# Optimization experiments

Hardware: AMD Instinct MI355X
Metric: run time of the kernel (lower is better)

The kernel has to match this reference:

```python
import math
import jax, jax.numpy as jnp
import numpy as np

B, N = 1, 512
C_S, C_Z, H, C, P_Q, P_V = 384, 128, 12, 16, 4, 8
CAT = C_Z * H + C * H + 3 * H * P_V + 1  # 2017


def _apply(t_r, t_t, x):
    # t_r: (b,n,3,3), t_t: (b,n,3), x: (b,3,h,p,n) -> global frame coords
    xg = jnp.einsum('bnij,bjhpn->bihpn', t_r, x)
    return xg + jnp.swapaxes(t_t, 1, 2)[:, :, None, None, :]


def setup_inputs() -> dict:
    key = jax.random.key(0)
    ks = jax.random.split(key, 14)
    f = lambda k, shp: jax.random.normal(k, shp, dtype=jnp.float32)
    return {
        's': f(ks[0], (B, C_S, N)),
        'z': f(ks[1], (B, C_Z, N, N)),
        't_r': f(ks[2], (B, N, 3, 3)),
        't_t': f(ks[3], (B, N, 3)),
        'Wq': f(ks[4], (C * H, C_S)) * 0.02,
        'Wk': f(ks[5], (C * H, C_S)) * 0.02,
        'Wv': f(ks[6], (C * H, C_S)) * 0.02,
        'Wqp': f(ks[7], (3 * H * P_Q, C_S)) * 0.02,
        'Wkp': f(ks[8], (3 * H * P_Q, C_S)) * 0.02,
        'Wvp': f(ks[9], (3 * H * P_V, C_S)) * 0.02,
        'Wb': f(ks[10], (H, C_Z)) * 0.02,
        'gamma': f(ks[11], (H, 1, 1)) * 0.5,
        'Ws': f(ks[12], (C_S, CAT)) * 0.02,
        'bs': jnp.zeros((C_S,), dtype=jnp.float32),
    }


def reference(s, z, t_r, t_t, Wq, Wk, Wv, Wqp, Wkp, Wvp, Wb, gamma, Ws, bs):
    b, _, n = s.shape
    w_c = math.sqrt(2.0 / (9.0 * P_Q))
    w_l = math.sqrt(1.0 / 3.0)

    proj = lambda W: jnp.einsum('oc,bcn->bon', W, s)
    # torch rearrange 'b (c h) i -> b c h i' == reshape(b, c, h, n)
    q = proj(Wq).reshape(b, C, H, n)
    k = proj(Wk).reshape(b, C, H, n)
    v = proj(Wv).reshape(b, C, H, n)
    qp = proj(Wqp).reshape(b, 3, H, P_Q, n)
    kp = proj(Wkp).reshape(b, 3, H, P_Q, n)
    vp = proj(Wvp).reshape(b, 3, H, P_V, n)

    qg = _apply(t_r, t_t, qp)  # (b,3,h,p,n)
    kg = _apply(t_r, t_t, kp)
    diff = qg[..., :, None] - kg[..., None, :]          # (b,3,h,p,n,n)
    dist2 = jnp.sum(diff * diff, axis=(1, 3))           # sum coords + points -> (b,h,n,n)
    tmp = jax.nn.softplus(gamma)[None] * (w_c / 2.0) * dist2

    b_bias = jnp.einsum('hc,bcij->bhij', Wb, z)
    qk = jnp.einsum('bchi,bchj->bhij', q, k) / math.sqrt(C)
    a = jax.nn.softmax(w_l * (qk + b_bias - tmp), axis=-1)  # (b,h,n,n)

    o1 = jnp.einsum('bhij,bcij->bchi', a, z).reshape(b, C_Z * H, n)
    o2 = jnp.einsum('bhij,bchj->bchi', a, v).reshape(b, C * H, n)

    vg = _apply(t_r, t_t, vp)                           # (b,3,h,pv,n)
    o3g = jnp.einsum('bhij,bchpj->bchpi', a, vg)        # (b,3,h,pv,n)
    t_r_inv = jnp.swapaxes(t_r, -1, -2)
    t_t_inv = jnp.einsum('bnij,bnj->bni', -t_r_inv, t_t)
    o3 = _apply(t_r_inv, t_t_inv, o3g).reshape(b, 3 * H * P_V, n)
    o3_norm = jnp.linalg.norm(o3, axis=1, keepdims=True)  # (b,1,n)

    cat = jnp.concatenate([o1, o2, o3, o3_norm], axis=1)  # (b, CAT, n)
    return jnp.einsum('oc,bcn->bon', Ws, cat) + bs[None, :, None]
```

## Files before the change

### kernel.cpp

```cpp
#include <hip/hip_runtime.h>
#include <math.h>

#define N 512
#define H 12
#define CC 16
#define CZ 128
#define CS 384
#define PQ 4
#define PV 8
#define CATR 2017

__global__ __launch_bounds__(256) void k_proj(
    const float* __restrict__ s,
    const float* __restrict__ Wq, const float* __restrict__ Wk, const float* __restrict__ Wv,
    const float* __restrict__ Wqp, const float* __restrict__ Wkp, const float* __restrict__ Wvp,
    float* __restrict__ proj)
{
    __shared__ float Wt[16][33];
    __shared__ float St[32][128];
    int t = threadIdx.x;
    int o0 = blockIdx.x * 16;
    int n0 = blockIdx.y * 128;
    const float* Wsrc; int orow;
    if (o0 < 192)      { Wsrc = Wq;  orow = o0; }
    else if (o0 < 384) { Wsrc = Wk;  orow = o0-192; }
    else if (o0 < 576) { Wsrc = Wv;  orow = o0-384; }
    else if (o0 < 720) { Wsrc = Wqp; orow = o0-576; }
    else if (o0 < 864) { Wsrc = Wkp; orow = o0-720; }
    else               { Wsrc = Wvp; orow = o0-864; }

    int og = t >> 6, nl = t & 63;
    float acc[4][2] = {};
    for (int c0 = 0; c0 < CS; c0 += 32) {
        __syncthreads();
        for (int k = 0; k < 2; k++) {
            int idx = t + k*256;
            int oo = idx >> 5, ccol = idx & 31;
            Wt[oo][ccol] = Wsrc[(orow+oo)*CS + c0 + ccol];
        }
        for (int k = 0; k < 4; k++) {
            int idx = t + k*256;
            int ccr = idx >> 5, nn4 = idx & 31;
            float4 v = *(const float4*)&s[(c0+ccr)*N + n0 + nn4*4];
            *(float4*)&St[ccr][nn4*4] = v;
        }
        __syncthreads();
        for (int kk = 0; kk < 32; kk++) {
            float sv0 = St[kk][nl], sv1 = St[kk][nl+64];
            #pragma unroll
            for (int r = 0; r < 4; r++) {
                float w = Wt[og*4+r][kk];
                acc[r][0] += w * sv0;
                acc[r][1] += w * sv1;
            }
        }
    }
    for (int r = 0; r < 4; r++) {
        int o = o0 + og*4 + r;
        proj[o*N + n0 + nl]      = acc[r][0];
        proj[o*N + n0 + 64 + nl] = acc[r][1];
    }
}

__global__ void k_frames(const float* __restrict__ proj,
                         const float* __restrict__ t_r, const float* __restrict__ t_t,
                         float* __restrict__ qg, float* __restrict__ kg, float* __restrict__ vg)
{
    int gid = blockIdx.x * blockDim.x + threadIdx.x;
    int n = gid & (N-1);
    int hp = gid >> 9;
    if (hp >= 192) return;
    const float* src; float* dst; int rowb, stride;
    if (hp < 48)      { src = proj + 576*N; dst = qg; rowb = hp;    stride = 48; }
    else if (hp < 96) { src = proj + 720*N; dst = kg; rowb = hp-48; stride = 48; }
    else              { src = proj + 864*N; dst = vg; rowb = hp-96; stride = 96; }
    float x0 = src[(rowb + 0*stride)*N + n];
    float x1 = src[(rowb + 1*stride)*N + n];
    float x2 = src[(rowb + 2*stride)*N + n];
    #pragma unroll
    for (int d = 0; d < 3; d++) {
        float r0 = t_r[(n*3+d)*3+0], r1 = t_r[(n*3+d)*3+1], r2 = t_r[(n*3+d)*3+2];
        dst[(rowb + d*stride)*N + n] = r0*x0 + r1*x1 + r2*x2 + t_t[n*3+d];
    }
}

__global__ void k_sq(const float* __restrict__ qg, const float* __restrict__ kg,
                     float* __restrict__ sq_q, float* __restrict__ sq_k)
{
    int gid = blockIdx.x * blockDim.x + threadIdx.x;
    int n = gid & (N-1);
    int sel = gid >> 9;
    int h = sel % H;
    const float* g = (sel < H) ? qg : kg;
    float* outp = (sel < H) ? sq_q : sq_k;
    float acc = 0.f;
    #pragma unroll
    for (int d = 0; d < 3; d++)
        #pragma unroll
        for (int p = 0; p < PQ; p++) {
            float v = g[(size_t)((d*H + h)*PQ + p)*N + n];
            acc += v*v;
        }
    outp[h*N + n] = acc;
}

__global__ __launch_bounds__(256) void k_logits(
    const float* __restrict__ z, const float* __restrict__ proj,
    const float* __restrict__ qg, const float* __restrict__ kg,
    const float* __restrict__ sq_q, const float* __restrict__ sq_k,
    const float* __restrict__ Wb, const float* __restrict__ gamma,
    float* __restrict__ a)
{
    __shared__ float red[12*2*256];
    int i = blockIdx.x;
    int jc = blockIdx.y;
    int t = threadIdx.x;
    int jl = t & 63;
    int cgu = __builtin_amdgcn_readfirstlane(t >> 6);
    int j = jc*256 + jl*4;
    const size_t NN = (size_t)N*N;
    const float w_l  = 0.57735026918962584f;
    const float w_c2 = 0.11785113019775793f;

    float ch[12];
    #pragma unroll
    for (int h = 0; h < 12; h++) {
        float g = gamma[h];
        float sp = (g > 20.f) ? g : log1pf(expf(g));
        ch[h] = sp * w_c2;
    }

    float acc[12][4] = {};

    {
        const float* zp = z + (size_t)(cgu*32)*NN + (size_t)i*N + j;
        for (int cc = 0; cc < 32; cc += 8) {
            float4 zb[8];
            #pragma unroll
            for (int u = 0; u < 8; u++)
                zb[u] = *(const float4*)(zp + (size_t)(cc+u)*NN);
            #pragma unroll
            for (int u = 0; u < 8; u++) {
                int c = cgu*32 + cc + u;
                #pragma unroll
                for (int h = 0; h < 12; h++) {
                    float w = Wb[h*CZ + c];
                    acc[h][0] += w*zb[u].x; acc[h][1] += w*zb[u].y;
                    acc[h][2] += w*zb[u].z; acc[h][3] += w*zb[u].w;
                }
            }
        }
    }
    {
        const float* q  = proj;
        const float* kk = proj + 192*N;
        #pragma unroll
        for (int cc = 0; cc < 4; cc++) {
            int c = cgu*4 + cc;
            #pragma unroll
            for (int h = 0; h < 12; h++) {
                int r = c*12 + h;
                float qv = 0.25f * q[(size_t)r*N + i];
                float4 k4 = *(const float4*)&kk[(size_t)r*N + j];
                acc[h][0] += qv*k4.x; acc[h][1] += qv*k4.y;
                acc[h][2] += qv*k4.z; acc[h][3] += qv*k4.w;
            }
        }
    }
    {
        #pragma unroll
        for (int dd = 0; dd < 3; dd++) {
            int dp = cgu*3 + dd; int d = dp >> 2, p = dp & 3;
            #pragma unroll
            for (int h = 0; h < 12; h++) {
                int r = (d*12 + h)*4 + p;
                float qv = 2.f * ch[h] * qg[(size_t)r*N + i];
                float4 k4 = *(const float4*)&kg[(size_t)r*N + j];
                acc[h][0] += qv*k4.x; acc[h][1] += qv*k4.y;
                acc[h][2] += qv*k4.z; acc[h][3] += qv*k4.w;
            }
        }
    }

    if (cgu >= 2) {
        #pragma unroll
        for (int h = 0; h < 12; h++) {
            float4 v; v.x=acc[h][0]; v.y=acc[h][1]; v.z=acc[h][2]; v.w=acc[h][3];
            *(float4*)&red[(h*2 + (cgu-2))*256 + jl*4] = v;
        }
    }
    __syncthreads();
    if (cgu < 2) {
        #pragma unroll
        for (int h = 0; h < 12; h++) {
            float4 o = *(const float4*)&red[(h*2 + cgu)*256 + jl*4];
            acc[h][0] += o.x; acc[h][1] += o.y; acc[h][2] += o.z; acc[h][3] += o.w;
        }
        if (cgu == 1) {
            #pragma unroll
            for (int h = 0; h < 12; h++) {
                float4 v; v.x=acc[h][0]; v.y=acc[h][1]; v.z=acc[h][2]; v.w=acc[h][3];
                *(float4*)&red[(h*2 + 1)*256 + jl*4] = v;
            }
        }
    }
    __syncthreads();
    if (cgu == 0) {
        #pragma unroll
        for (int h = 0; h < 12; h++) {
            float4 o = *(const float4*)&red[(h*2 + 1)*256 + jl*4];
            float s0 = sq_q[h*N + i];
            float4 sk = *(const float4*)&sq_k[h*N + j];
            float4 r;
            r.x = w_l*(acc[h][0] + o.x - ch[h]*(s0 + sk.x));
            r.y = w_l*(acc[h][1] + o.y - ch[h]*(s0 + sk.y));
            r.z = w_l*(acc[h][2] + o.z - ch[h]*(s0 + sk.z));
            r.w = w_l*(acc[h][3] + o.w - ch[h]*(s0 + sk.w));
            *(float4*)&a[((size_t)h*N + i)*N + j] = r;
        }
    }
}

__global__ __launch_bounds__(256) void k_softmax(float* __restrict__ a)
{
    int r = blockIdx.x*4 + (threadIdx.x >> 6);
    int l = threadIdx.x & 63;
    float* row = a + (size_t)r*N + l*8;
    float4 v0 = *(const float4*)row;
    float4 v1 = *(const float4*)(row + 4);
    float m = fmaxf(fmaxf(fmaxf(v0.x,v0.y),fmaxf(v0.z,v0.w)),
                    fmaxf(fmaxf(v1.x,v1.y),fmaxf(v1.z,v1.w)));
    for (int s = 32; s > 0; s >>= 1) m = fmaxf(m, __shfl_xor(m, s));
    v0.x = __expf(v0.x-m); v0.y = __expf(v0.y-m);
    v0.z = __expf(v0.z-m); v0.w = __expf(v0.w-m);
    v1.x = __expf(v1.x-m); v1.y = __expf(v1.y-m);
    v1.z = __expf(v1.z-m); v1.w = __expf(v1.w-m);
    float sm = v0.x+v0.y+v0.z+v0.w+v1.x+v1.y+v1.z+v1.w;
    for (int s = 32; s > 0; s >>= 1) sm += __shfl_xor(sm, s);
    float inv = 1.f/sm;
    v0.x*=inv; v0.y*=inv; v0.z*=inv; v0.w*=inv;
    v1.x*=inv; v1.y*=inv; v1.z*=inv; v1.w*=inv;
    *(float4*)row = v0;
    *(float4*)(row+4) = v1;
}

__global__ __launch_bounds__(256) void k_o1(
    const float* __restrict__ z, const float* __restrict__ a, float* __restrict__ cat)
{
    __shared__ float als[12*516];
    __shared__ float zls[64*68];
    int i = blockIdx.x;
    int c0 = blockIdx.y * 64;
    int t = threadIdx.x;
    int cg = t & 31, hg = (t>>5)&1, jq = t>>6;

    #pragma unroll
    for (int k = 0; k < 6; k++) {
        int idx = t + k*256;
        int h = idx >> 7, j4 = idx & 127;
        *(float4*)&als[h*516 + j4*4] = *(const float4*)&a[((size_t)h*N + i)*N + j4*4];
    }
    float acc[2][6] = {};
    for (int jc = 0; jc < 8; jc++) {
        __syncthreads();
        #pragma unroll
        for (int k = 0; k < 4; k++) {
            int idx = t + k*256;
            int c = idx >> 4, j4 = idx & 15;
            *(float4*)&zls[c*68 + j4*4] =
                *(const float4*)&z[((size_t)(c0+c)*N + i)*N + jc*64 + j4*4];
        }
        __syncthreads();
        #pragma unroll
        for (int s = 0; s < 4; s++) {
            int jo = jq*16 + s*4;
            float4 z0 = *(const float4*)&zls[cg*68 + jo];
            float4 z1 = *(const float4*)&zls[(cg+32)*68 + jo];
            #pragma unroll
            for (int hh = 0; hh < 6; hh++) {
                float4 a4 = *(const float4*)&als[(hg*6+hh)*516 + jc*64 + jo];
                acc[0][hh] += z0.x*a4.x + z0.y*a4.y + z0.z*a4.z + z0.w*a4.w;
                acc[1][hh] += z1.x*a4.x + z1.y*a4.y + z1.z*a4.z + z1.w*a4.w;
            }
        }
    }
    __syncthreads();
    if (jq >= 2) {
        float* rb = &zls[((jq-2)*128 + (t & 127))*13];
        #pragma unroll
        for (int r = 0; r < 2; r++)
            #pragma unroll
            for (int hh = 0; hh < 6; hh++) rb[r*6+hh] = acc[r][hh];
    }
    __syncthreads();
    if (jq < 2) {
        const float* rb = &zls[(jq*128 + (t & 127))*13];
        #pragma unroll
        for (int r = 0; r < 2; r++)
            #pragma unroll
            for (int hh = 0; hh < 6; hh++) acc[r][hh] += rb[r*6+hh];
        if (jq == 1) {
            float* rb2 = &als[(t & 63)*13];
            #pragma unroll
            for (int r = 0; r < 2; r++)
                #pragma unroll
                for (int hh = 0; hh < 6; hh++) rb2[r*6+hh] = acc[r][hh];
        }
    }
    __syncthreads();
    if (jq == 0) {
        const float* rb2 = &als[t*13];
        #pragma unroll
        for (int r = 0; r < 2; r++)
            #pragma unroll
            for (int hh = 0; hh < 6; hh++) {
                float v = acc[r][hh] + rb2[r*6+hh];
                int c = c0 + cg + 32*r;
                int h = hg*6 + hh;
                cat[(size_t)(c*H + h)*N + i] = v;
            }
    }
}

__global__ __launch_bounds__(256) void k_o2o3g(
    const float* __restrict__ a, const float* __restrict__ proj, const float* __restrict__ vg,
    float* __restrict__ cat, float* __restrict__ o3g)
{
    __shared__ float ats[8*132];
    __shared__ float vts[40*132];
    int h = blockIdx.x, i0 = blockIdx.y*8;
    int t = threadIdx.x;
    int il = t & 7, rg = (t>>3)&7, jq = t>>6;
    const float* v = proj + 384*N;
    float acc[5] = {};
    for (int jc = 0; jc < 4; jc++) {
        __syncthreads();
        {
            int ii = t >> 5, j4 = t & 31;
            *(float4*)&ats[ii*132 + j4*4] =
                *(const float4*)&a[((size_t)h*N + i0+ii)*N + jc*128 + j4*4];
        }
        #pragma unroll
        for (int k = 0; k < 5; k++) {
            int idx = t + k*256;
            int r = idx >> 5, j4 = idx & 31;
            const float* src = (r < 16) ? (v + (size_t)(r*H + h)*N)
                : (vg + (size_t)(((r-16)>>3)*96 + h*PV + ((r-16)&7))*N);
            *(float4*)&vts[r*132 + j4*4] = *(const float4*)&src[jc*128 + j4*4];
        }
        __syncthreads();
        #pragma unroll
        for (int s = 0; s < 8; s++) {
            int jo = jq*32 + s*4;
            float4 a4 = *(const float4*)&ats[il*132 + jo];
            #pragma unroll
            for (int r = 0; r < 5; r++) {
                float4 v4 = *(const float4*)&vts[(rg*5+r)*132 + jo];
                acc[r] += v4.x*a4.x + v4.y*a4.y + v4.z*a4.z + v4.w*a4.w;
            }
        }
    }
    __syncthreads();
    if (jq >= 2) {
        float* rb = &ats[((jq-2)*64 + (t & 63))*5];
        #pragma unroll
        for (int r = 0; r < 5; r++) rb[r] = acc[r];
    }
    __syncthreads();
    if (jq < 2) {
        const float* rb = &ats[(jq*64 + (t & 63))*5];
        #pragma unroll
        for (int r = 0; r < 5; r++) acc[r] += rb[r];
        if (jq == 1) {
            float* rb2 = &ats[640 + (t & 63)*5];
            #pragma unroll
            for (int r = 0; r < 5; r++) rb2[r] = acc[r];
        }
    }
    __syncthreads();
    if (jq == 0) {
        const float* rb2 = &ats[640 + t*5];
        #pragma unroll
        for (int r = 0; r < 5; r++) {
            float val = acc[r] + rb2[r];
            int row = rg*5 + r;
            if (row < 16) cat[(size_t)(1536 + row*H + h)*N + i0 + il] = val;
            else { int rr = row - 16;
                   o3g[(size_t)((rr>>3)*96 + h*PV + (rr&7))*N + i0 + il] = val; }
        }
    }
}

__global__ void k_o3(const float* __restrict__ o3g,
                     const float* __restrict__ t_r, const float* __restrict__ t_t,
                     float* __restrict__ cat)
{
    int gid = blockIdx.x*blockDim.x + threadIdx.x;
    int i = gid & (N-1), hp = gid >> 9;
    if (hp >= 96) return;
    float x0 = o3g[(size_t)(0*96 + hp)*N + i] - t_t[i*3+0];
    float x1 = o3g[(size_t)(1*96 + hp)*N + i] - t_t[i*3+1];
    float x2 = o3g[(size_t)(2*96 + hp)*N + i] - t_t[i*3+2];
    #pragma unroll
    for (int d = 0; d < 3; d++) {
        float o = t_r[(i*3+0)*3+d]*x0 + t_r[(i*3+1)*3+d]*x1 + t_r[(i*3+2)*3+d]*x2;
        cat[(size_t)(1728 + d*96 + hp)*N + i] = o;
    }
}

__global__ void k_norm(float* __restrict__ cat)
{
    int i = blockIdx.x*blockDim.x + threadIdx.x;
    if (i >= N) return;
    float acc = 0.f;
    for (int r = 0; r < 288; r++) {
        float v = cat[(size_t)(1728+r)*N + i];
        acc += v*v;
    }
    cat[(size_t)2016*N + i] = sqrtf(acc);
}

__global__ __launch_bounds__(256) void k_final(
    const float* __restrict__ Ws, const float* __restrict__ bs,
    const float* __restrict__ cat, float* __restrict__ out)
{
    __shared__ float Wt[16*33];
    __shared__ float Ct[32*66];
    int o0 = blockIdx.x*16, n0 = blockIdx.y*64;
    int ks = blockIdx.z;
    int kbeg = ks*505, kend = min(CATR, kbeg+505);
    int t = threadIdx.x;
    int og = t >> 6, nl = t & 63;
    float acc[4] = {};
    for (int c0 = kbeg; c0 < kend; c0 += 32) {
        __syncthreads();
        for (int k = 0; k < 2; k++) {
            int idx = t + k*256;
            int oo = idx >> 5, ccol = idx & 31;
            int c = c0 + ccol;
            Wt[oo*33 + ccol] = (c < kend) ? Ws[(size_t)(o0+oo)*CATR + c] : 0.f;
        }
        for (int k = 0; k < 4; k++) {
            int idx = t + k*256;
            int ccr = idx >> 5, j2 = idx & 31;
            int c = c0 + ccr;
            float2 vv; vv.x = 0.f; vv.y = 0.f;
            if (c < kend) vv = *(const float2*)&cat[(size_t)c*N + n0 + j2*2];
            *(float2*)&Ct[ccr*66 + j2*2] = vv;
        }
        __syncthreads();
        int klim = min(32, kend - c0);
        for (int kk = 0; kk < klim; kk++) {
            float cv = Ct[kk*66 + nl];
            #pragma unroll
            for (int r = 0; r < 4; r++)
                acc[r] += Wt[(og*4+r)*33 + kk] * cv;
        }
    }
    #pragma unroll
    for (int r = 0; r < 4; r++) {
        int o = o0 + og*4 + r;
        float val = acc[r];
        if (ks == 0) val += bs[o];
        atomicAdd(&out[(size_t)o*N + n0 + nl], val);
    }
}

extern "C" void kernel_launch(void* const* d_in, const int* in_sizes, int n_in,
                              void* d_out, int out_size, void* d_ws, size_t ws_size,
                              hipStream_t stream)
{
    const float* s     = (const float*)d_in[0];
    const float* z     = (const float*)d_in[1];
    const float* t_r   = (const float*)d_in[2];
    const float* t_t   = (const float*)d_in[3];
    const float* Wq    = (const float*)d_in[4];
    const float* Wk    = (const float*)d_in[5];
    const float* Wv    = (const float*)d_in[6];
    const float* Wqp   = (const float*)d_in[7];
    const float* Wkp   = (const float*)d_in[8];
    const float* Wvp   = (const float*)d_in[9];
    const float* Wb    = (const float*)d_in[10];
    const float* gamma = (const float*)d_in[11];
    const float* Ws    = (const float*)d_in[12];
    const float* bs    = (const float*)d_in[13];
    float* out = (float*)d_out;

    float* ws   = (float*)d_ws;
    float* proj = ws;
    float* qg   = proj + 1152*N;
    float* kg   = qg   + 144*N;
    float* vg   = kg   + 144*N;
    float* sq_q = vg   + 288*N;
    float* sq_k = sq_q + H*N;
    float* o3g  = sq_k + H*N;
    float* a    = o3g  + 288*N;
    float* cat  = a    + (size_t)H*N*N;

    k_proj   <<<dim3(72,4),   256, 0, stream>>>(s, Wq, Wk, Wv, Wqp, Wkp, Wvp, proj);
    k_frames <<<384,          256, 0, stream>>>(proj, t_r, t_t, qg, kg, vg);
    k_sq     <<<48,           256, 0, stream>>>(qg, kg, sq_q, sq_k);
    k_logits <<<dim3(512,2),  256, 0, stream>>>(z, proj, qg, kg, sq_q, sq_k, Wb, gamma, a);
    k_softmax<<<1536,         256, 0, stream>>>(a);
    k_o1     <<<dim3(512,2),  256, 0, stream>>>(z, a, cat);
    k_o2o3g  <<<dim3(12,64),  256, 0, stream>>>(a, proj, vg, cat, o3g);
    k_o3     <<<192,          256, 0, stream>>>(o3g, t_r, t_t, cat);
    k_norm   <<<2,            256, 0, stream>>>(cat);
    hipMemsetAsync(out, 0, (size_t)CS*N*sizeof(float), stream);
    k_final  <<<dim3(24,8,4), 256, 0, stream>>>(Ws, bs, cat, out);
}
```

Baseline: 418.2 us.

## Fuse logits, softmax and z-weighted output into one per-row kernel

```diff
diff --git a/kernel.cpp b/kernel.cpp
--- a/kernel.cpp
+++ b/kernel.cpp
@@ -104,20 +104,19 @@
     outp[h*N + n] = acc;
 }
 
-__global__ __launch_bounds__(256) void k_logits(
+__global__ __launch_bounds__(256) void k_attn_o1(
     const float* __restrict__ z, const float* __restrict__ proj,
     const float* __restrict__ qg, const float* __restrict__ kg,
     const float* __restrict__ sq_q, const float* __restrict__ sq_k,
     const float* __restrict__ Wb, const float* __restrict__ gamma,
-    float* __restrict__ a)
-{
-    __shared__ float red[12*2*256];
+    float* __restrict__ a, float* __restrict__ cat)
+{
+    __shared__ float als[12*516];
+    __shared__ float zls[128*68];
     int i = blockIdx.x;
-    int jc = blockIdx.y;
     int t = threadIdx.x;
     int jl = t & 63;
     int cgu = __builtin_amdgcn_readfirstlane(t >> 6);
-    int j = jc*256 + jl*4;
     const size_t NN = (size_t)N*N;
     const float w_l  = 0.57735026918962584f;
     const float w_c2 = 0.11785113019775793f;
@@ -130,192 +129,189 @@
         ch[h] = sp * w_c2;
     }
 
-    float acc[12][4] = {};
-
-    {
-        const float* zp = z + (size_t)(cgu*32)*NN + (size_t)i*N + j;
-        for (int cc = 0; cc < 32; cc += 8) {
-            float4 zb[8];
-            #pragma unroll
-            for (int u = 0; u < 8; u++)
-                zb[u] = *(const float4*)(zp + (size_t)(cc+u)*NN);
-            #pragma unroll
-            for (int u = 0; u < 8; u++) {
-                int c = cgu*32 + cc + u;
+    for (int jc = 0; jc < 2; jc++) {
+        int j = jc*256 + jl*4;
+        float acc[12][4] = {};
+
+        {
+            const float* zp = z + (size_t)(cgu*32)*NN + (size_t)i*N + j;
+            for (int cc = 0; cc < 32; cc += 8) {
+                float4 zb[8];
+                #pragma unroll
+                for (int u = 0; u < 8; u++)
+                    zb[u] = *(const float4*)(zp + (size_t)(cc+u)*NN);
+                #pragma unroll
+                for (int u = 0; u < 8; u++) {
+                    int c = cgu*32 + cc + u;
+                    #pragma unroll
+                    for (int h = 0; h < 12; h++) {
+                        float w = Wb[h*CZ + c];
+                        acc[h][0] += w*zb[u].x; acc[h][1] += w*zb[u].y;
+                        acc[h][2] += w*zb[u].z; acc[h][3] += w*zb[u].w;
+                    }
+                }
+            }
+        }
+        {
+            const float* q  = proj;
+            const float* kk = proj + 192*N;
+            #pragma unroll
+            for (int cc = 0; cc < 4; cc++) {
+                int c = cgu*4 + cc;
                 #pragma unroll
                 for (int h = 0; h < 12; h++) {
-                    float w = Wb[h*CZ + c];
-                    acc[h][0] += w*zb[u].x; acc[h][1] += w*zb[u].y;
-                    acc[h][2] += w*zb[u].z; acc[h][3] += w*zb[u].w;
+                    int r = c*12 + h;
+                    float qv = 0.25f * q[(size_t)r*N + i];
+                    float4 k4 = *(const float4*)&kk[(size_t)r*N + j];
+                    acc[h][0] += qv*k4.x; acc[h][1] += qv*k4.y;
+                    acc[h][2] += qv*k4.z; acc[h][3] += qv*k4.w;
                 }
             }
         }
-    }
-    {
-        const float* q  = proj;
-        const float* kk = proj + 192*N;
-        #pragma unroll
-        for (int cc = 0; cc < 4; cc++) {
-            int c = cgu*4 + cc;
-            #pragma unroll
-            for (int h = 0; h < 12; h++) {
-                int r = c*12 + h;
-                float qv = 0.25f * q[(size_t)r*N + i];
-                float4 k4 = *(const float4*)&kk[(size_t)r*N + j];
-                acc[h][0] += qv*k4.x; acc[h][1] += qv*k4.y;
-                acc[h][2] += qv*k4.z; acc[h][3] += qv*k4.w;
-            }
-        }
-    }
-    {
-        #pragma unroll
-        for (int dd = 0; dd < 3; dd++) {
-            int dp = cgu*3 + dd; int d = dp >> 2, p = dp & 3;
-            #pragma unroll
-            for (int h = 0; h < 12; h++) {
-                int r = (d*12 + h)*4 + p;
-                float qv = 2.f * ch[h] * qg[(size_t)r*N + i];
-                float4 k4 = *(const float4*)&kg[(size_t)r*N + j];
-                acc[h][0] += qv*k4.x; acc[h][1] += qv*k4.y;
-                acc[h][2] += qv*k4.z; acc[h][3] += qv*k4.w;
-            }
-        }
-    }
-
-    if (cgu >= 2) {
-        #pragma unroll
-        for (int h = 0; h < 12; h++) {
-            float4 v; v.x=acc[h][0]; v.y=acc[h][1]; v.z=acc[h][2]; v.w=acc[h][3];
-            *(float4*)&red[(h*2 + (cgu-2))*256 + jl*4] = v;
-        }
-    }
-    __syncthreads();
-    if (cgu < 2) {
-        #pragma unroll
-        for (int h = 0; h < 12; h++) {
-            float4 o = *(const float4*)&red[(h*2 + cgu)*256 + jl*4];
-            acc[h][0] += o.x; acc[h][1] += o.y; acc[h][2] += o.z; acc[h][3] += o.w;
-        }
-        if (cgu == 1) {
+        {
+            #pragma unroll
+            for (int dd = 0; dd < 3; dd++) {
+                int dp = cgu*3 + dd; int d = dp >> 2, p = dp & 3;
+                #pragma unroll
+                for (int h = 0; h < 12; h++) {
+                    int r = (d*12 + h)*4 + p;
+                    float qv = 2.f * ch[h] * qg[(size_t)r*N + i];
+                    float4 k4 = *(const float4*)&kg[(size_t)r*N + j];
+                    acc[h][0] += qv*k4.x; acc[h][1] += qv*k4.y;
+                    acc[h][2] += qv*k4.z; acc[h][3] += qv*k4.w;
+                }
+            }
+        }
+
+        __syncthreads();
+        float* red = zls;
+        if (cgu >= 2) {
             #pragma unroll
             for (int h = 0; h < 12; h++) {
                 float4 v; v.x=acc[h][0]; v.y=acc[h][1]; v.z=acc[h][2]; v.w=acc[h][3];
-                *(float4*)&red[(h*2 + 1)*256 + jl*4] = v;
-            }
-        }
-    }
-    __syncthreads();
-    if (cgu == 0) {
-        #pragma unroll
-        for (int h = 0; h < 12; h++) {
-            float4 o = *(const float4*)&red[(h*2 + 1)*256 + jl*4];
-            float s0 = sq_q[h*N + i];
-            float4 sk = *(const float4*)&sq_k[h*N + j];
-            float4 r;
-            r.x = w_l*(acc[h][0] + o.x - ch[h]*(s0 + sk.x));
-            r.y = w_l*(acc[h][1] + o.y - ch[h]*(s0 + sk.y));
-            r.z = w_l*(acc[h][2] + o.z - ch[h]*(s0 + sk.z));
-            r.w = w_l*(acc[h][3] + o.w - ch[h]*(s0 + sk.w));
-            *(float4*)&a[((size_t)h*N + i)*N + j] = r;
-        }
-    }
-}
-
-__global__ __launch_bounds__(256) void k_softmax(float* __restrict__ a)
-{
-    int r = blockIdx.x*4 + (threadIdx.x >> 6);
-    int l = threadIdx.x & 63;
-    float* row = a + (size_t)r*N + l*8;
-    float4 v0 = *(const float4*)row;
-    float4 v1 = *(const float4*)(row + 4);
-    float m = fmaxf(fmaxf(fmaxf(v0.x,v0.y),fmaxf(v0.z,v0.w)),
-                    fmaxf(fmaxf(v1.x,v1.y),fmaxf(v1.z,v1.w)));
-    for (int s = 32; s > 0; s >>= 1) m = fmaxf(m, __shfl_xor(m, s));
-    v0.x = __expf(v0.x-m); v0.y = __expf(v0.y-m);
-    v0.z = __expf(v0.z-m); v0.w = __expf(v0.w-m);
-    v1.x = __expf(v1.x-m); v1.y = __expf(v1.y-m);
-    v1.z = __expf(v1.z-m); v1.w = __expf(v1.w-m);
-    float sm = v0.x+v0.y+v0.z+v0.w+v1.x+v1.y+v1.z+v1.w;
-    for (int s = 32; s > 0; s >>= 1) sm += __shfl_xor(sm, s);
-    float inv = 1.f/sm;
-    v0.x*=inv; v0.y*=inv; v0.z*=inv; v0.w*=inv;
-    v1.x*=inv; v1.y*=inv; v1.z*=inv; v1.w*=inv;
-    *(float4*)row = v0;
-    *(float4*)(row+4) = v1;
-}
-
-__global__ __launch_bounds__(256) void k_o1(
-    const float* __restrict__ z, const float* __restrict__ a, float* __restrict__ cat)
-{
-    __shared__ float als[12*516];
-    __shared__ float zls[64*68];
-    int i = blockIdx.x;
-    int c0 = blockIdx.y * 64;
-    int t = threadIdx.x;
+                *(float4*)&red[(h*2 + (cgu-2))*256 + jl*4] = v;
+            }
+        }
+        __syncthreads();
+        if (cgu < 2) {
+            #pragma unroll
+            for (int h = 0; h < 12; h++) {
+                float4 o = *(const float4*)&red[(h*2 + cgu)*256 + jl*4];
+                acc[h][0] += o.x; acc[h][1] += o.y; acc[h][2] += o.z; acc[h][3] += o.w;
+            }
+            if (cgu == 1) {
+                #pragma unroll
+                for (int h = 0; h < 12; h++) {
+                    float4 v; v.x=acc[h][0]; v.y=acc[h][1]; v.z=acc[h][2]; v.w=acc[h][3];
+                    *(float4*)&red[(h*2 + 1)*256 + jl*4] = v;
+                }
+            }
+        }
+        __syncthreads();
+        if (cgu == 0) {
+            #pragma unroll
+            for (int h = 0; h < 12; h++) {
+                float4 o = *(const float4*)&red[(h*2 + 1)*256 + jl*4];
+                float s0 = sq_q[h*N + i];
+                float4 sk = *(const float4*)&sq_k[h*N + j];
+                float4 r;
+                r.x = w_l*(acc[h][0] + o.x - ch[h]*(s0 + sk.x));
+                r.y = w_l*(acc[h][1] + o.y - ch[h]*(s0 + sk.y));
+                r.z = w_l*(acc[h][2] + o.z - ch[h]*(s0 + sk.z));
+                r.w = w_l*(acc[h][3] + o.w - ch[h]*(s0 + sk.w));
+                *(float4*)&als[h*516 + jc*256 + jl*4] = r;
+            }
+        }
+    }
+    __syncthreads();
+
+    #pragma unroll
+    for (int hh = 0; hh < 3; hh++) {
+        int h = cgu*3 + hh;
+        float* row = &als[h*516 + jl*8];
+        float4 v0 = *(const float4*)row;
+        float4 v1 = *(const float4*)(row+4);
+        float m = fmaxf(fmaxf(fmaxf(v0.x,v0.y),fmaxf(v0.z,v0.w)),
+                        fmaxf(fmaxf(v1.x,v1.y),fmaxf(v1.z,v1.w)));
+        for (int s = 32; s > 0; s >>= 1) m = fmaxf(m, __shfl_xor(m, s));
+        v0.x = __expf(v0.x-m); v0.y = __expf(v0.y-m);
+        v0.z = __expf(v0.z-m); v0.w = __expf(v0.w-m);
+        v1.x = __expf(v1.x-m); v1.y = __expf(v1.y-m);
+        v1.z = __expf(v1.z-m); v1.w = __expf(v1.w-m);
+        float sm = v0.x+v0.y+v0.z+v0.w+v1.x+v1.y+v1.z+v1.w;
+        for (int s = 32; s > 0; s >>= 1) sm += __shfl_xor(sm, s);
+        float inv = 1.f/sm;
+        v0.x*=inv; v0.y*=inv; v0.z*=inv; v0.w*=inv;
+        v1.x*=inv; v1.y*=inv; v1.z*=inv; v1.w*=inv;
+        *(float4*)row = v0;
+        *(float4*)(row+4) = v1;
+        float* garow = &a[((size_t)h*N + i)*N + jl*8];
+        *(float4*)garow = v0;
+        *(float4*)(garow+4) = v1;
+    }
+    __syncthreads();
+
     int cg = t & 31, hg = (t>>5)&1, jq = t>>6;
-
-    #pragma unroll
-    for (int k = 0; k < 6; k++) {
-        int idx = t + k*256;
-        int h = idx >> 7, j4 = idx & 127;
-        *(float4*)&als[h*516 + j4*4] = *(const float4*)&a[((size_t)h*N + i)*N + j4*4];
-    }
-    float acc[2][6] = {};
+    float acc[4][6] = {};
     for (int jc = 0; jc < 8; jc++) {
         __syncthreads();
         #pragma unroll
-        for (int k = 0; k < 4; k++) {
+        for (int k = 0; k < 8; k++) {
             int idx = t + k*256;
             int c = idx >> 4, j4 = idx & 15;
             *(float4*)&zls[c*68 + j4*4] =
-                *(const float4*)&z[((size_t)(c0+c)*N + i)*N + jc*64 + j4*4];
+                *(const float4*)&z[((size_t)c*N + i)*N + jc*64 + j4*4];
         }
         __syncthreads();
         #pragma unroll
         for (int s = 0; s < 4; s++) {
             int jo = jq*16 + s*4;
-            float4 z0 = *(const float4*)&zls[cg*68 + jo];
-            float4 z1 = *(const float4*)&zls[(cg+32)*68 + jo];
-            #pragma unroll
-            for (int hh = 0; hh < 6; hh++) {
-                float4 a4 = *(const float4*)&als[(hg*6+hh)*516 + jc*64 + jo];
-                acc[0][hh] += z0.x*a4.x + z0.y*a4.y + z0.z*a4.z + z0.w*a4.w;
-                acc[1][hh] += z1.x*a4.x + z1.y*a4.y + z1.z*a4.z + z1.w*a4.w;
+            float4 a4[6];
+            #pragma unroll
+            for (int hh = 0; hh < 6; hh++)
+                a4[hh] = *(const float4*)&als[(hg*6+hh)*516 + jc*64 + jo];
+            #pragma unroll
+            for (int r = 0; r < 4; r++) {
+                float4 zz = *(const float4*)&zls[(cg + 32*r)*68 + jo];
+                #pragma unroll
+                for (int hh = 0; hh < 6; hh++)
+                    acc[r][hh] += zz.x*a4[hh].x + zz.y*a4[hh].y
+                                + zz.z*a4[hh].z + zz.w*a4[hh].w;
             }
         }
     }
     __syncthreads();
     if (jq >= 2) {
-        float* rb = &zls[((jq-2)*128 + (t & 127))*13];
-        #pragma unroll
-        for (int r = 0; r < 2; r++)
+        float* rb = &zls[((jq-2)*128 + (t & 127))*25];
+        #pragma unroll
+        for (int r = 0; r < 4; r++)
             #pragma unroll
             for (int hh = 0; hh < 6; hh++) rb[r*6+hh] = acc[r][hh];
     }
     __syncthreads();
     if (jq < 2) {
-        const float* rb = &zls[(jq*128 + (t & 127))*13];
-        #pragma unroll
-        for (int r = 0; r < 2; r++)
+        const float* rb = &zls[(jq*128 + (t & 127))*25];
+        #pragma unroll
+        for (int r = 0; r < 4; r++)
             #pragma unroll
             for (int hh = 0; hh < 6; hh++) acc[r][hh] += rb[r*6+hh];
         if (jq == 1) {
-            float* rb2 = &als[(t & 63)*13];
-            #pragma unroll
-            for (int r = 0; r < 2; r++)
+            float* rb2 = &als[(t & 63)*25];
+            #pragma unroll
+            for (int r = 0; r < 4; r++)
                 #pragma unroll
                 for (int hh = 0; hh < 6; hh++) rb2[r*6+hh] = acc[r][hh];
         }
     }
     __syncthreads();
     if (jq == 0) {
-        const float* rb2 = &als[t*13];
-        #pragma unroll
-        for (int r = 0; r < 2; r++)
+        const float* rb2 = &als[t*25];
+        #pragma unroll
+        for (int r = 0; r < 4; r++)
             #pragma unroll
             for (int hh = 0; hh < 6; hh++) {
                 float v = acc[r][hh] + rb2[r*6+hh];
-                int c = c0 + cg + 32*r;
+                int c = cg + 32*r;
                 int h = hg*6 + hh;
                 cat[(size_t)(c*H + h)*N + i] = v;
             }
@@ -500,9 +496,7 @@
     k_proj   <<<dim3(72,4),   256, 0, stream>>>(s, Wq, Wk, Wv, Wqp, Wkp, Wvp, proj);
     k_frames <<<384,          256, 0, stream>>>(proj, t_r, t_t, qg, kg, vg);
     k_sq     <<<48,           256, 0, stream>>>(qg, kg, sq_q, sq_k);
-    k_logits <<<dim3(512,2),  256, 0, stream>>>(z, proj, qg, kg, sq_q, sq_k, Wb, gamma, a);
-    k_softmax<<<1536,         256, 0, stream>>>(a);
-    k_o1     <<<dim3(512,2),  256, 0, stream>>>(z, a, cat);
+    k_attn_o1<<<512,          256, 0, stream>>>(z, proj, qg, kg, sq_q, sq_k, Wb, gamma, a, cat);
     k_o2o3g  <<<dim3(12,64),  256, 0, stream>>>(a, proj, vg, cat, o3g);
     k_o3     <<<192,          256, 0, stream>>>(o3g, t_r, t_t, cat);
     k_norm   <<<2,            256, 0, stream>>>(cat);
```

Measured after the change: 410.4 us. Within noise of the previous version (-1.9%).
